# Performance work log

Measured on AMD Instinct MI355X. Metric: run time of the kernel, lower is better.

The kernel has to match this reference:

```python
import jax, jax.numpy as jnp
import numpy as np

B, S, LW = 128, 256, 20          # batch, sent len, max word len
VW, VC = 400000, 80              # word / char vocab
DC, DW, HC, HW, NT = 25, 300, 25, 200, 10  # dims from args.dims; NT tags
DIN = DW + 2 * HC                # word-LSTM input dim = 350


def setup_inputs() -> dict:
    key = jax.random.key(0)
    ks = jax.random.split(key, 16)
    s = 0.1
    return {
        "words_batch": jax.random.randint(ks[0], (B, S), 0, VW),
        "chars_batch": jax.random.randint(ks[1], (B, S, LW), 0, VC),
        "lens_word": jnp.sort(jax.random.randint(ks[2], (B,), 1, S + 1))[::-1],
        "emb_char": jax.random.normal(ks[3], (VC + 1, DC), jnp.float32) * s,
        "emb_word": jax.random.normal(ks[4], (VW, DW), jnp.float32) * s,
        "conv_w": jax.random.normal(ks[5], (2 * HC, 1, 3, DC), jnp.float32) * s,
        "conv_b": jnp.zeros((2 * HC,), jnp.float32),
        "w_ih_f": jax.random.normal(ks[6], (4 * HW, DIN), jnp.float32) * s,
        "w_hh_f": jax.random.normal(ks[7], (4 * HW, HW), jnp.float32) * s,
        "b_f": jnp.zeros((4 * HW,), jnp.float32),
        "w_ih_b": jax.random.normal(ks[8], (4 * HW, DIN), jnp.float32) * s,
        "w_hh_b": jax.random.normal(ks[9], (4 * HW, HW), jnp.float32) * s,
        "b_b": jnp.zeros((4 * HW,), jnp.float32),
        "proj_w": jax.random.normal(ks[10], (NT, 2 * HW), jnp.float32) * s,
        "proj_b": jnp.zeros((NT,), jnp.float32),
    }


def _lstm_dir(xg, w_hh, mask, reverse):
    # xg: [S,B,4H] precomputed input-gate contributions; mask: [S,B,1]
    Hh = w_hh.shape[1]
    h0 = jnp.zeros((xg.shape[1], Hh), xg.dtype)
    c0 = jnp.zeros_like(h0)

    def step(carry, inp):
        h, c = carry
        xg_t, m = inp
        g = xg_t + h @ w_hh.T
        i, f, gg, o = jnp.split(g, 4, axis=-1)
        i, f, o = jax.nn.sigmoid(i), jax.nn.sigmoid(f), jax.nn.sigmoid(o)
        gg = jnp.tanh(gg)
        c_new = f * c + i * gg
        h_new = o * jnp.tanh(c_new)
        h = jnp.where(m, h_new, h)
        c = jnp.where(m, c_new, c)
        out = jnp.where(m, h_new, 0.0)  # pad_packed zeros beyond length
        return (h, c), out

    _, out = jax.lax.scan(step, (h0, c0), (xg, mask), reverse=reverse)
    return out  # [S,B,H]


def reference(words_batch, chars_batch, lens_word, emb_char, emb_word,
              conv_w, conv_b, w_ih_f, w_hh_f, b_f, w_ih_b, w_hh_b, b_b,
              proj_w, proj_b):
    # --- char CNN encoder ---
    ec = emb_char[chars_batch]                       # [B,S,LW,DC]
    x = ec.reshape(B * S, 1, LW, DC)
    y = jax.lax.conv_general_dilated(x, conv_w, (1, 1), [(2, 2), (0, 0)])
    y = y + conv_b[None, :, None, None]              # [B*S, 2HC, LW+2, 1]
    out_char = y.max(axis=(2, 3)).reshape(B, S, 2 * HC)
    # --- word features ---
    ew = emb_word[words_batch]                       # [B,S,DW]
    feats = jnp.concatenate([ew, out_char], axis=-1) # [B,S,DIN]
    # --- masked BiLSTM over words (packed-sequence semantics) ---
    mask = (jnp.arange(S)[None, :] < lens_word[:, None])  # [B,S]
    mask_t = mask.T[:, :, None]                      # [S,B,1]
    xf = jnp.einsum('bsd,gd->sbg', feats, w_ih_f) + b_f
    xb = jnp.einsum('bsd,gd->sbg', feats, w_ih_b) + b_b
    hf = _lstm_dir(xf, w_hh_f, mask_t, reverse=False)
    hb = _lstm_dir(xb, w_hh_b, mask_t, reverse=True)
    enc = jnp.concatenate([hf, hb], axis=-1).transpose(1, 0, 2)  # [B,S,2HW]
    # --- emissions ---
    return jnp.einsum('bsh,th->bst', enc, proj_w) + proj_b       # [B,S,NT]
```

## Files before the change

kernel.cpp:

```cpp
#include <hip/hip_runtime.h>

typedef unsigned short u16;
typedef __attribute__((ext_vector_type(4))) unsigned short u16x4;
typedef __attribute__((ext_vector_type(8))) short bf16x8;
typedef __attribute__((ext_vector_type(4))) float f32x4;

#define BB 128
#define SS 256
#define LWW 20
#define NTg 10
#define HWg 200
#define G4 800
#define DWg 300
#define DIN 350
#define KP 352
#define NP 896
#define NW (BB*SS)
#define OUTN (NW*NTg)

__device__ __forceinline__ float b2f(u16 u){ return __uint_as_float(((unsigned)u)<<16); }
__device__ __forceinline__ u16 f2b(float f){
  unsigned x = __float_as_uint(f);
  unsigned r = (x + 0x7fffu + ((x>>16)&1u)) >> 16;
  return (u16)r;
}
__device__ __forceinline__ float ldf(const void* p, long long i, int isb){
  return isb ? b2f(((const u16*)p)[i]) : ((const float*)p)[i];
}
__device__ __forceinline__ int ldi(const void* p, long long i, int i64){
  return i64 ? (int)((const long long*)p)[i] : ((const int*)p)[i];
}
__device__ __forceinline__ f32x4 mfma16(bf16x8 a, bf16x8 b, f32x4 c){
  return __builtin_amdgcn_mfma_f32_16x16x32_bf16(a,b,c,0,0,0);
}
__device__ __forceinline__ float sigf(float x){
  return __builtin_amdgcn_rcpf(1.f + __expf(-x));
}
__device__ __forceinline__ float tanhf_(float x){
  return 1.f - 2.f*__builtin_amdgcn_rcpf(1.f + __expf(2.f*x));
}

__global__ void k_diag(float* out, float code){
  int i = blockIdx.x*256 + threadIdx.x;
  if(i<OUTN) out[i]=code;
}

__global__ void k_probe(const void* p, int* flag){
  __shared__ int cnt;
  if(threadIdx.x==0) cnt=0;
  __syncthreads();
  float a = fabsf(b2f(((const u16*)p)[threadIdx.x]));
  if(a>1e-5f && a<1.0f) atomicAdd(&cnt,1);
  __syncthreads();
  if(threadIdx.x==0) *flag = (cnt>=100)?1:0;
}
__global__ void k_probe_int(const int* __restrict__ words, int* iflag){
  __shared__ int zc;
  if(threadIdx.x==0) zc=0;
  __syncthreads();
  int z=0;
  for(int k=threadIdx.x;k<128;k+=64)
    if(words[2*k+1]==0) z++;
  atomicAdd(&zc,z);
  __syncthreads();
  if(threadIdx.x==0) *iflag = (zc>=100)?1:0;
}

__global__ void k_stage_wih(const void* __restrict__ src, u16* __restrict__ dst,
                            const int* __restrict__ flag){
  int isb=*flag;
  int i = blockIdx.x*256 + threadIdx.x;
  if(i>=NP*KP) return;
  int n=i/KP, k=i-n*KP;
  float v = (n<G4 && k<DIN) ? ldf(src,(long long)n*DIN+k,isb) : 0.f;
  dst[i]=f2b(v);
}
__global__ void k_stage_whh(const void* __restrict__ src, u16* __restrict__ dst,
                            const int* __restrict__ flag){
  int isb=*flag;
  int i = blockIdx.x*256 + threadIdx.x;
  if(i>=179200) return;
  int tile=i/3584, r=i%3584, ks=r/512, r2=r%512, l=r2/8, j=r2%8;
  int n=tile*16+(l&15), k=ks*32+((l>>4)<<3)+j;
  float v = (k<HWg)? ldf(src,(long long)n*HWg+k,isb) : 0.f;
  dst[i]=f2b(v);
}
__global__ void k_stage_misc(const void* echar, const void* convw, const void* cb,
                             const void* bfp, const void* bbp, const void* pw, const void* pb,
                             float* d_ec, float* d_cw, float* d_cb,
                             float* d_bf, float* d_bb, float* d_pw, float* d_pb,
                             const int* __restrict__ flag){
  int isb=*flag;
  int i = blockIdx.x*256 + threadIdx.x;
  if(i<2025){ d_ec[i]=ldf(echar,i,isb); return; } i-=2025;
  if(i<3750){ d_cw[i]=ldf(convw,i,isb); return; } i-=3750;
  if(i<64){ d_cb[i]=(i<50)?ldf(cb,i,isb):0.f; return; } i-=64;
  if(i<800){ d_bf[i]=ldf(bfp,i,isb); return; } i-=800;
  if(i<800){ d_bb[i]=ldf(bbp,i,isb); return; } i-=800;
  if(i<4000){ d_pw[i]=ldf(pw,i,isb); return; } i-=4000;
  if(i<16){ d_pb[i]=(i<10)?ldf(pb,i,isb):0.f; return; }
}

__global__ void k_gather(const void* __restrict__ words, const void* __restrict__ embw,
                         u16* __restrict__ feats,
                         const int* __restrict__ flag, const int* __restrict__ iflag){
  int isb=*flag, i64=*iflag;
  int wv=threadIdx.x>>6, lane=threadIdx.x&63;
  int row = blockIdx.x*4 + wv;
  int idx = ldi(words,row,i64);
  u16* d = feats + (size_t)row*KP;
  if(isb){
    const u16* s=(const u16*)embw + (long long)idx*DWg;
    for(int c=lane;c<DWg;c+=64) d[c]=s[c];
  } else {
    const float* s=(const float*)embw + (long long)idx*DWg;
    for(int c=lane;c<DWg;c+=64) d[c]=f2b(s[c]);
  }
  if(lane<2) d[350+lane]=0;
}

__global__ __launch_bounds__(256) void k_char(const void* __restrict__ chars,
                      const float* __restrict__ ec, const float* __restrict__ cw,
                      const float* __restrict__ cb, u16* __restrict__ feats,
                      const int* __restrict__ iflag){
  int i64=*iflag;
  int gid = blockIdx.x*256 + threadIdx.x;
  int w = gid/50, f = gid - w*50;
  int ch[20];
  #pragma unroll
  for(int r=0;r<20;r++) ch[r]=ldi(chars,(long long)w*LWW+r,i64);
  float acc[22];
  #pragma unroll
  for(int t=0;t<22;t++) acc[t]=0.f;
  for(int c=0;c<25;c++){
    float wv0=cw[(f*3+0)*25+c];
    float wv1=cw[(f*3+1)*25+c];
    float wv2=cw[(f*3+2)*25+c];
    #pragma unroll
    for(int r=0;r<20;r++){
      float xv = ec[ch[r]*25+c];
      acc[r+2] += xv*wv0;
      acc[r+1] += xv*wv1;
      acc[r]   += xv*wv2;
    }
  }
  float m=-1e30f;
  #pragma unroll
  for(int t=0;t<22;t++) m=fmaxf(m,acc[t]);
  feats[(size_t)w*KP + 300 + f] = f2b(m + cb[f]);
}

__global__ __launch_bounds__(256) void k_gemm(const u16* __restrict__ feats,
                      const u16* __restrict__ wih, const float* __restrict__ bias,
                      u16* __restrict__ xg){
  __shared__ u16 At[128*40];
  __shared__ u16 Bt[128*40];
  int tid=threadIdx.x, m0=blockIdx.x*128, n0=blockIdx.y*128;
  int wv=tid>>6, lane=tid&63;
  int wr=(wv>>1)*64, wc=(wv&1)*64;
  const f32x4 z4={0.f,0.f,0.f,0.f};
  f32x4 acc[4][4];
  #pragma unroll
  for(int a=0;a<4;a++){ acc[a][0]=z4; acc[a][1]=z4; acc[a][2]=z4; acc[a][3]=z4; }
  int row=tid>>2, grp=tid&3;
  for(int kt=0;kt<11;kt++){
    int k0=kt*32;
    #pragma unroll
    for(int p=0;p<2;p++){
      int r=row+p*64;
      *(int4*)&At[r*40+grp*8] = *(const int4*)&feats[(size_t)(m0+r)*KP + k0 + grp*8];
      *(int4*)&Bt[r*40+grp*8] = *(const int4*)&wih  [(size_t)(n0+r)*KP + k0 + grp*8];
    }
    __syncthreads();
    bf16x8 af[4], bg[4];
    #pragma unroll
    for(int ri=0;ri<4;ri++) af[ri]=*(const bf16x8*)&At[(wr+ri*16+(lane&15))*40 + ((lane>>4)<<3)];
    #pragma unroll
    for(int ni=0;ni<4;ni++) bg[ni]=*(const bf16x8*)&Bt[(wc+ni*16+(lane&15))*40 + ((lane>>4)<<3)];
    #pragma unroll
    for(int ri=0;ri<4;ri++)
      #pragma unroll
      for(int ni=0;ni<4;ni++) acc[ri][ni]=mfma16(af[ri],bg[ni],acc[ri][ni]);
    __syncthreads();
  }
  #pragma unroll
  for(int ni=0;ni<4;ni++){
    int n = n0 + wc + ni*16 + (lane&15);
    if(n>=G4) continue;
    float bv = bias[n];
    int g4=n/200, j=n-g4*200;
    #pragma unroll
    for(int ri=0;ri<4;ri++)
      #pragma unroll
      for(int rr=0;rr<4;rr++){
        int m = m0 + wr + ri*16 + ((lane>>4)&3)*4 + rr;
        int b = m>>8, s = m&255;
        xg[((size_t)s*BB + b)*G4 + j*4 + g4] = f2b(acc[ri][ni][rr] + bv);
      }
  }
}

__global__ __launch_bounds__(512,1) void k_lstm(
    const u16* __restrict__ xgf, const u16* __restrict__ xgb,
    const u16* __restrict__ whhf, const u16* __restrict__ whhb,
    const void* __restrict__ lens, u16* __restrict__ enc,
    const int* __restrict__ iflag)
{
  extern __shared__ char smem[];
  float* g_buf = (float*)smem;
  u16*  h_b   = (u16*)(smem + 51456);
  int*  len_s = (int*)(smem + 51456 + 7424);
  u16*  wlds  = (u16*)(smem + 51456 + 7424 + 64);

  const int blk=blockIdx.x, dir=blk&1, b0=(blk>>1)*16;
  const u16* xg  = dir? xgb : xgf;
  const u16* whh = dir? whhb : whhf;
  const int tid=threadIdx.x, wv=tid>>6, lane=tid&63;
  const int i64=*iflag;

  for(int i=tid;i<16*232;i+=512) h_b[i]=0;
  if(tid<16) len_s[tid]=ldi(lens,b0+tid,i64);
  for(int i=tid;i<7168;i+=512) wlds[i]=whh[48*3584 + i];

  bf16x8 wf[6][7];
  #pragma unroll
  for(int i=0;i<6;i++)
    #pragma unroll
    for(int ks=0;ks<7;ks++)
      wf[i][ks]=*(const bf16x8*)&whh[(size_t)((wv*6+i)*7+ks)*512 + lane*8];

  int q[7], jj[7]; float c[7];
  #pragma unroll
  for(int k=0;k<7;k++){
    int e=tid+512*k; if(e>3199) e=3199;
    q[k]=e/200; jj[k]=e-q[k]*200; c[k]=0.f;
  }
  __syncthreads();
  int lenv[7];
  #pragma unroll
  for(int k=0;k<7;k++) lenv[k]=len_s[q[k]];

  const f32x4 z4={0.f,0.f,0.f,0.f};
  for(int step=0; step<SS; ++step){
    const int t = dir ? (SS-1-step) : step;
    const u16* xgt = xg + (size_t)t*(BB*G4);
    u16x4 xr[7];
    #pragma unroll
    for(int k=0;k<7;k++)
      if(tid+512*k<3200) xr[k]=*(const u16x4*)&xgt[(size_t)(b0+q[k])*G4 + jj[k]*4];

    f32x4 acc[6], acc7=z4;
    #pragma unroll
    for(int i=0;i<6;i++) acc[i]=z4;
    #pragma unroll
    for(int ks=0;ks<7;ks++){
      bf16x8 a=*(const bf16x8*)&h_b[(lane&15)*232 + ks*32 + ((lane>>4)<<3)];
      #pragma unroll
      for(int i=0;i<6;i++) acc[i]=mfma16(a,wf[i][ks],acc[i]);
      if(wv<2){
        bf16x8 bw=*(const bf16x8*)&wlds[(wv*7+ks)*512 + lane*8];
        acc7=mfma16(a,bw,acc7);
      }
    }
    #pragma unroll
    for(int i=0;i<6;i++){
      int col=(wv*6+i)*16+(lane&15);
      #pragma unroll
      for(int rr=0;rr<4;rr++) g_buf[(((lane>>4)&3)*4+rr)*804 + col]=acc[i][rr];
    }
    if(wv<2){
      int col=(48+wv)*16+(lane&15);
      #pragma unroll
      for(int rr=0;rr<4;rr++) g_buf[(((lane>>4)&3)*4+rr)*804 + col]=acc7[rr];
    }
    __syncthreads();
    #pragma unroll
    for(int k=0;k<7;k++){
      if(tid+512*k<3200){
        const int qq=q[k], j=jj[k];
        float gi=g_buf[qq*804 + j      ] + b2f(xr[k].x);
        float gf=g_buf[qq*804 + 200 + j] + b2f(xr[k].y);
        float gg=g_buf[qq*804 + 400 + j] + b2f(xr[k].z);
        float go=g_buf[qq*804 + 600 + j] + b2f(xr[k].w);
        float iv=sigf(gi), fv=sigf(gf), gv=tanhf_(gg), ov=sigf(go);
        float cn=fv*c[k] + iv*gv;
        float hn=ov*tanhf_(cn);
        const bool m = t < lenv[k];
        enc[((size_t)(b0+qq)*SS + t)*(2*HWg) + dir*HWg + j] = m ? f2b(hn) : (u16)0;
        if(m){ c[k]=cn; h_b[qq*232 + j]=f2b(hn); }
      }
    }
    __syncthreads();
  }
}

__global__ __launch_bounds__(256) void k_emis(const u16* __restrict__ enc,
                      const float* __restrict__ pw_g, const float* __restrict__ pb,
                      float* __restrict__ out){
  __shared__ float pw[10*404];
  int tid=threadIdx.x;
  for(int i=tid;i<4000;i+=256){ int tg=i/400,h=i-tg*400; pw[tg*404+h]=pw_g[i]; }
  __syncthreads();
  int idx = blockIdx.x*256 + tid;
  int bs = idx/NTg, tg = idx-bs*NTg;
  const u16* er = enc + (size_t)bs*(2*HWg);
  float acc=0.f;
  #pragma unroll 4
  for(int h=0;h<400;h+=4){
    u16x4 v=*(const u16x4*)&er[h];
    acc += b2f(v.x)*pw[tg*404+h]   + b2f(v.y)*pw[tg*404+h+1]
         + b2f(v.z)*pw[tg*404+h+2] + b2f(v.w)*pw[tg*404+h+3];
  }
  out[idx] = acc + pb[tg];
}

extern "C" void kernel_launch(void* const* d_in, const int* in_sizes, int n_in,
                              void* d_out, int out_size, void* d_ws, size_t ws_size,
                              hipStream_t stream){
  float* out=(float*)d_out;
  if(n_in!=15){ k_diag<<<1280,256,0,stream>>>(out, 20480.f); return; }
  if(out_size!=OUTN){ k_diag<<<1280,256,0,stream>>>(out, 24576.f); return; }

  const void* words=d_in[0];
  const void* chars=d_in[1];
  const void* lens =d_in[2];
  const void* echar=d_in[3];
  const void* embw =d_in[4];
  const void* convw=d_in[5];
  const void* convb=d_in[6];
  const void* wihf =d_in[7];
  const void* whhf =d_in[8];
  const void* bfp  =d_in[9];
  const void* wihb =d_in[10];
  const void* whhb =d_in[11];
  const void* bbp  =d_in[12];
  const void* pw   =d_in[13];
  const void* pb   =d_in[14];

  char* ws=(char*)d_ws;
  size_t cur=0;
  auto alloc=[&](size_t sz){ size_t o=cur; cur=(cur+sz+255)&~(size_t)255; return o; };
  size_t oF    = alloc(4);
  size_t oIF   = alloc(4);
  size_t oWIHF = alloc((size_t)NP*KP*2);
  size_t oWIHB = alloc((size_t)NP*KP*2);
  size_t oWHHF = alloc(179200*2);
  size_t oWHHB = alloc(179200*2);
  size_t oEC   = alloc(2025*4);
  size_t oCW   = alloc(3750*4);
  size_t oCB   = alloc(64*4);
  size_t oBF   = alloc(800*4);
  size_t oBB   = alloc(800*4);
  size_t oPW   = alloc(4000*4);
  size_t oPB   = alloc(16*4);
  size_t oSH   = alloc((size_t)NW*2*HWg*2);
  size_t oXGF  = alloc((size_t)SS*BB*G4*2);
  size_t oXGB  = alloc((size_t)SS*BB*G4*2);
  size_t need  = cur;

  if(ws_size < need){
    k_diag<<<1280,256,0,stream>>>(out, 16384.f + 64.f*(float)(ws_size>>20));
    return;
  }

  int*   flag =(int*)(ws+oF);
  int*   iflag=(int*)(ws+oIF);
  u16*   sWIHF=(u16*)(ws+oWIHF);
  u16*   sWIHB=(u16*)(ws+oWIHB);
  u16*   sWHHF=(u16*)(ws+oWHHF);
  u16*   sWHHB=(u16*)(ws+oWHHB);
  float* sEC  =(float*)(ws+oEC);
  float* sCW  =(float*)(ws+oCW);
  float* sCB  =(float*)(ws+oCB);
  float* sBF  =(float*)(ws+oBF);
  float* sBB  =(float*)(ws+oBB);
  float* sPW  =(float*)(ws+oPW);
  float* sPB  =(float*)(ws+oPB);
  u16*   feats=(u16*)(ws+oSH);
  u16*   enc  =(u16*)(ws+oSH);
  u16*   xgfp =(u16*)(ws+oXGF);
  u16*   xgbp =(u16*)(ws+oXGB);

  k_probe<<<1,128,0,stream>>>(embw, flag);
  k_probe_int<<<1,64,0,stream>>>((const int*)words, iflag);
  k_stage_wih<<<1232,256,0,stream>>>(wihf, sWIHF, flag);
  k_stage_wih<<<1232,256,0,stream>>>(wihb, sWIHB, flag);
  k_stage_whh<<<700,256,0,stream>>>(whhf, sWHHF, flag);
  k_stage_whh<<<700,256,0,stream>>>(whhb, sWHHB, flag);
  k_stage_misc<<<45,256,0,stream>>>(echar, convw, convb, bfp, bbp, pw, pb,
                                    sEC, sCW, sCB, sBF, sBB, sPW, sPB, flag);
  k_gather<<<8192,256,0,stream>>>(words, embw, feats, flag, iflag);
  k_char<<<6400,256,0,stream>>>(chars, sEC, sCW, sCB, feats, iflag);
  k_gemm<<<dim3(256,7),256,0,stream>>>(feats, sWIHF, sBF, xgfp);
  k_gemm<<<dim3(256,7),256,0,stream>>>(feats, sWIHB, sBB, xgbp);
  k_lstm<<<16,512,73280,stream>>>(xgfp, xgbp, sWHHF, sWHHB, lens, enc, iflag);
  k_emis<<<1280,256,0,stream>>>(enc, sPW, sPB, out);
}
```

Before: 1.846 ms.

## Interleave LSTM gate columns so cell update runs on MFMA registers

Recurrent weights are re-staged so that each 16-column MFMA tile holds the four gates of the same hidden units interleaved. Lane shuffles then gather the gates in registers, so the gate values no longer make a round trip through a shared-memory buffer. The hidden state is double-buffered, which leaves one barrier per timestep instead of two. The next step's input-gate values are prefetched while the current step is computed. The shuffle logic and the new weight layout must stay consistent with the MFMA output layout.

```diff
diff --git a/kernel.cpp b/kernel.cpp
--- a/kernel.cpp
+++ b/kernel.cpp
@@ -80,8 +80,11 @@
   int isb=*flag;
   int i = blockIdx.x*256 + threadIdx.x;
   if(i>=179200) return;
-  int tile=i/3584, r=i%3584, ks=r/512, r2=r%512, l=r2/8, j=r2%8;
-  int n=tile*16+(l&15), k=ks*32+((l>>4)<<3)+j;
+  int tile=i/3584, r=i%3584, ks=r/512, r2=r%512, l=r2/8, jreg=r2%8;
+  int c = tile*16 + (l&15);
+  int j = c>>2, gate = c&3;
+  int n = gate*200 + j;
+  int k = ks*32 + ((l>>4)<<3) + jreg;
   float v = (k<HWg)? ldf(src,(long long)n*HWg+k,isb) : 0.f;
   dst[i]=f2b(v);
 }
@@ -200,17 +203,39 @@
   }
 }
 
+__device__ __forceinline__ void lstm_upd(int lane, int t, int lenv,
+    f32x4 a, u16x4 xrv, float& cstv, float& hregv,
+    u16* __restrict__ enc, int eoffv, u16* hnp, int hboffv){
+  float v0=a[0], v1=a[1], v2=a[2], v3=a[3];
+  float f0,f1,r0,r1;
+  const bool hi2=(lane&2)!=0;
+  f0 = hi2? v0:v2; f1 = hi2? v1:v3;
+  r0=__shfl_xor(f0,2); r1=__shfl_xor(f1,2);
+  if(hi2){v0=r0;v1=r1;} else {v2=r0;v3=r1;}
+  const bool hi1=(lane&1)!=0;
+  f0 = hi1? v0:v1; f1 = hi1? v2:v3;
+  r0=__shfl_xor(f0,1); r1=__shfl_xor(f1,1);
+  if(hi1){v0=r0;v2=r1;} else {v1=r0;v3=r1;}
+  float gi=v0+b2f(xrv.x), gf=v1+b2f(xrv.y);
+  float gg=v2+b2f(xrv.z), go=v3+b2f(xrv.w);
+  float iv=sigf(gi), fv=sigf(gf), gv=tanhf_(gg), ov=sigf(go);
+  float cn=fv*cstv+iv*gv;
+  float hv=ov*tanhf_(cn);
+  const bool m = t<lenv;
+  if(m){ cstv=cn; hregv=hv; }
+  enc[(size_t)eoffv + (size_t)t*(2*HWg)] = m? f2b(hv):(u16)0;
+  hnp[hboffv] = f2b(hregv);
+}
+
 __global__ __launch_bounds__(512,1) void k_lstm(
     const u16* __restrict__ xgf, const u16* __restrict__ xgb,
     const u16* __restrict__ whhf, const u16* __restrict__ whhb,
     const void* __restrict__ lens, u16* __restrict__ enc,
     const int* __restrict__ iflag)
 {
-  extern __shared__ char smem[];
-  float* g_buf = (float*)smem;
-  u16*  h_b   = (u16*)(smem + 51456);
-  int*  len_s = (int*)(smem + 51456 + 7424);
-  u16*  wlds  = (u16*)(smem + 51456 + 7424 + 64);
+  __shared__ u16 hbuf[2][16*232];
+  __shared__ int len_s[16];
+  __shared__ u16 wlds[7168];
 
   const int blk=blockIdx.x, dir=blk&1, b0=(blk>>1)*16;
   const u16* xg  = dir? xgb : xgf;
@@ -218,7 +243,7 @@
   const int tid=threadIdx.x, wv=tid>>6, lane=tid&63;
   const int i64=*iflag;
 
-  for(int i=tid;i<16*232;i+=512) h_b[i]=0;
+  for(int i=tid;i<2*16*232;i+=512) ((u16*)hbuf)[i]=0;
   if(tid<16) len_s[tid]=ldi(lens,b0+tid,i64);
   for(int i=tid;i<7168;i+=512) wlds[i]=whh[48*3584 + i];
 
@@ -229,68 +254,77 @@
     for(int ks=0;ks<7;ks++)
       wf[i][ks]=*(const bf16x8*)&whh[(size_t)((wv*6+i)*7+ks)*512 + lane*8];
 
-  int q[7], jj[7]; float c[7];
-  #pragma unroll
-  for(int k=0;k<7;k++){
-    int e=tid+512*k; if(e>3199) e=3199;
-    q[k]=e/200; jj[k]=e-q[k]*200; c[k]=0.f;
-  }
-  __syncthreads();
-  int lenv[7];
-  #pragma unroll
-  for(int k=0;k<7;k++) lenv[k]=len_s[q[k]];
+  const int bl = ((lane>>4)<<2) + (lane&3);
+  const int jl = (lane>>2)&3;
+  __syncthreads();
+  const int lenv = len_s[bl];
+
+  int xoff[7], eoff[7], hboff[7];
+  #pragma unroll
+  for(int q=0;q<6;q++){
+    int j=(wv*6+q)*4+jl;
+    xoff[q]=(b0+bl)*G4 + j*4;
+    eoff[q]=((b0+bl)*SS)*(2*HWg) + dir*HWg + j;
+    hboff[q]=bl*232 + j;
+  }
+  { int j=(48+wv)*4+jl;
+    xoff[6]=(b0+bl)*G4 + j*4;
+    eoff[6]=((b0+bl)*SS)*(2*HWg) + dir*HWg + j;
+    hboff[6]=bl*232 + j; }
+
+  float cst[7]={0,0,0,0,0,0,0}, hreg[7]={0,0,0,0,0,0,0};
+  u16x4 xr[7];
+  {
+    const int t0 = dir? (SS-1):0;
+    const size_t tb=(size_t)t0*(BB*G4);
+    #pragma unroll
+    for(int q=0;q<6;q++) xr[q]=*(const u16x4*)&xg[tb+xoff[q]];
+    if(wv<2) xr[6]=*(const u16x4*)&xg[tb+xoff[6]];
+  }
 
   const f32x4 z4={0.f,0.f,0.f,0.f};
+  int cur=0;
   for(int step=0; step<SS; ++step){
     const int t = dir ? (SS-1-step) : step;
-    const u16* xgt = xg + (size_t)t*(BB*G4);
-    u16x4 xr[7];
-    #pragma unroll
-    for(int k=0;k<7;k++)
-      if(tid+512*k<3200) xr[k]=*(const u16x4*)&xgt[(size_t)(b0+q[k])*G4 + jj[k]*4];
-
-    f32x4 acc[6], acc7=z4;
-    #pragma unroll
-    for(int i=0;i<6;i++) acc[i]=z4;
-    #pragma unroll
-    for(int ks=0;ks<7;ks++){
-      bf16x8 a=*(const bf16x8*)&h_b[(lane&15)*232 + ks*32 + ((lane>>4)<<3)];
+    int sn = step+1; if(sn>SS-1) sn=SS-1;
+    const int tn = dir ? (SS-1-sn) : sn;
+    const size_t tbn=(size_t)tn*(BB*G4);
+    const u16* hc = hbuf[cur];
+    u16* hn_ = hbuf[cur^1];
+
+    bf16x8 afr[7];
+    #pragma unroll
+    for(int ks=0;ks<7;ks++)
+      afr[ks]=*(const bf16x8*)&hc[(lane&15)*232 + ks*32 + ((lane>>4)<<3)];
+
+    f32x4 acc[7];
+    #pragma unroll
+    for(int i=0;i<6;i++){
+      acc[i]=z4;
       #pragma unroll
-      for(int i=0;i<6;i++) acc[i]=mfma16(a,wf[i][ks],acc[i]);
-      if(wv<2){
+      for(int ks=0;ks<7;ks++) acc[i]=mfma16(afr[ks],wf[i][ks],acc[i]);
+    }
+    acc[6]=z4;
+    if(wv<2){
+      #pragma unroll
+      for(int ks=0;ks<7;ks++){
         bf16x8 bw=*(const bf16x8*)&wlds[(wv*7+ks)*512 + lane*8];
-        acc7=mfma16(a,bw,acc7);
+        acc[6]=mfma16(afr[ks],bw,acc[6]);
       }
     }
-    #pragma unroll
-    for(int i=0;i<6;i++){
-      int col=(wv*6+i)*16+(lane&15);
-      #pragma unroll
-      for(int rr=0;rr<4;rr++) g_buf[(((lane>>4)&3)*4+rr)*804 + col]=acc[i][rr];
+
+    #pragma unroll
+    for(int q=0;q<6;q++){
+      lstm_upd(lane,t,lenv,acc[q],xr[q],cst[q],hreg[q],enc,eoff[q],hn_,hboff[q]);
+      xr[q]=*(const u16x4*)&xg[tbn+xoff[q]];
     }
     if(wv<2){
-      int col=(48+wv)*16+(lane&15);
-      #pragma unroll
-      for(int rr=0;rr<4;rr++) g_buf[(((lane>>4)&3)*4+rr)*804 + col]=acc7[rr];
-    }
+      lstm_upd(lane,t,lenv,acc[6],xr[6],cst[6],hreg[6],enc,eoff[6],hn_,hboff[6]);
+      xr[6]=*(const u16x4*)&xg[tbn+xoff[6]];
+    }
+
     __syncthreads();
-    #pragma unroll
-    for(int k=0;k<7;k++){
-      if(tid+512*k<3200){
-        const int qq=q[k], j=jj[k];
-        float gi=g_buf[qq*804 + j      ] + b2f(xr[k].x);
-        float gf=g_buf[qq*804 + 200 + j] + b2f(xr[k].y);
-        float gg=g_buf[qq*804 + 400 + j] + b2f(xr[k].z);
-        float go=g_buf[qq*804 + 600 + j] + b2f(xr[k].w);
-        float iv=sigf(gi), fv=sigf(gf), gv=tanhf_(gg), ov=sigf(go);
-        float cn=fv*c[k] + iv*gv;
-        float hn=ov*tanhf_(cn);
-        const bool m = t < lenv[k];
-        enc[((size_t)(b0+qq)*SS + t)*(2*HWg) + dir*HWg + j] = m ? f2b(hn) : (u16)0;
-        if(m){ c[k]=cn; h_b[qq*232 + j]=f2b(hn); }
-      }
-    }
-    __syncthreads();
+    cur^=1;
   }
 }
 
@@ -393,6 +427,6 @@
   k_char<<<6400,256,0,stream>>>(chars, sEC, sCW, sCB, feats, iflag);
   k_gemm<<<dim3(256,7),256,0,stream>>>(feats, sWIHF, sBF, xgfp);
   k_gemm<<<dim3(256,7),256,0,stream>>>(feats, sWIHB, sBB, xgbp);
-  k_lstm<<<16,512,73280,stream>>>(xgfp, xgbp, sWHHF, sWHHB, lens, enc, iflag);
+  k_lstm<<<16,512,0,stream>>>(xgfp, xgbp, sWHHF, sWHHB, lens, enc, iflag);
   k_emis<<<1280,256,0,stream>>>(enc, sPW, sPB, out);
 }
```

Result: faster. 1.615 ms (-12.5%).
